# Performance work log

Hardware: AMD Instinct MI355X
Metric: run time of the kernel (lower is better)

The kernel has to match this reference:

```python
import jax, jax.numpy as jnp
import numpy as np

N, D, R, C_IN = 384, 256, 64, 2
REL_H, NEI_H = 128, 256


def setup_inputs() -> dict:
    key = jax.random.key(0)
    ks = jax.random.split(key, 16)
    inp = {
        "corr_index": jax.random.normal(ks[0], (N, N, C_IN), jnp.float32),
        "nei_index": jax.random.randint(ks[1], (N, N), 0, 2, jnp.int32),
        "nei_num": jax.random.randint(ks[2], (N,), 0, N, jnp.int32),
        "outgate": jax.random.uniform(ks[3], (N, D), jnp.float32),
        "self_h": jax.random.normal(ks[4], (N, D), jnp.float32),
        "self_c": jax.random.normal(ks[5], (N, D), jnp.float32),
        # relativeLayer: 2-layer MLP, relu after both layers (iflastac=True)
        "rel_w1": jax.random.normal(ks[6], (C_IN, REL_H), jnp.float32) * 0.1,
        "rel_b1": jnp.zeros((REL_H,), jnp.float32),
        "rel_w2": jax.random.normal(ks[7], (REL_H, R), jnp.float32) * 0.1,
        "rel_b2": jnp.zeros((R,), jnp.float32),
        # ngate: single Linear(R+2D -> D) + sigmoid
        "ngate_w": jax.random.normal(ks[8], (R + 2 * D, D), jnp.float32) * 0.005,
        "ngate_b": jnp.zeros((D,), jnp.float32),
        # WAr: single Linear(R+2D -> 1), no activation (WAr_ac='')
        "war_w": jax.random.normal(ks[9], (R + 2 * D, 1), jnp.float32) * 0.05,
        "war_b": jnp.zeros((1,), jnp.float32),
        # W_nei: Linear(D->NEI_H)+relu, Linear(NEI_H->D), no last activation
        "wnei_w1": jax.random.normal(ks[10], (D, NEI_H), jnp.float32) * 0.05,
        "wnei_b1": jnp.zeros((NEI_H,), jnp.float32),
        "wnei_w2": jax.random.normal(ks[11], (NEI_H, D), jnp.float32) * 0.05,
        "wnei_b2": jnp.zeros((D,), jnp.float32),
    }
    return inp


def reference(corr_index, nei_index, nei_num, outgate, self_h, self_c,
              rel_w1, rel_b1, rel_w2, rel_b2, ngate_w, ngate_b,
              war_w, war_b, wnei_w1, wnei_b1, wnei_w2, wnei_b2):
    n, d = self_h.shape
    mask = nei_index > 0  # [N, N], pair (i, j)
    # relativeLayer on pairwise relative coords: relu(relu(x W1 + b1) W2 + b2)
    r = jax.nn.relu(jax.nn.relu(corr_index @ rel_w1 + rel_b1) @ rel_w2 + rel_b2)  # [N,N,R]
    # In torch code flat index k = i*N + j: hi_t[k] = self_h[i], nei_inputs[k] = self_h[j]
    h_i = jnp.broadcast_to(self_h[:, None, :], (n, n, d))
    h_j = jnp.broadcast_to(self_h[None, :, :], (n, n, d))
    feat = jnp.concatenate([r, h_i, h_j], axis=-1)  # [N,N,R+2D]
    gate = jax.nn.sigmoid(feat @ ngate_w + ngate_b)  # [N,N,D]
    msg = h_j * gate
    tt = (feat @ war_w + war_b)[..., 0]  # [N,N] attention logits
    # scatter into zero-init matrix, then Pos[Pos==0] = -inf, row softmax
    pos = jnp.where(mask, tt, 0.0)
    pos = jnp.where(pos == 0.0, -jnp.inf, pos)
    pos = jax.nn.softmax(pos, axis=1)  # [N,N]
    # masked, attention-weighted messages; guard NaN from fully-masked rows
    H = jnp.where(mask[:, :, None], msg * pos[:, :, None], 0.0)  # [N,N,D]
    h_sum = jnp.sum(H, axis=1)  # [N,D]
    h_sum = jax.nn.relu(h_sum @ wnei_w1 + wnei_b1) @ wnei_w2 + wnei_b2
    C = h_sum + self_c
    H_out = outgate * jnp.tanh(C)
    return (outgate, H_out, C)
```

## Files before the change

kernel.cpp:

```cpp
#include <hip/hip_runtime.h>
#include <hip/hip_bf16.h>
#include <math.h>

#define N 384
#define D 256
#define R 64
#define RELH 128
#define NN (N*N)
#define ND (N*D)
#define JCHUNK 64
#define NCHUNK (N / JCHUNK)
#define TPB 16
#define LOG2E 1.44269504088896f

typedef _Float16 f16x8 __attribute__((ext_vector_type(8)));
typedef float f32x4 __attribute__((ext_vector_type(4)));

__device__ __forceinline__ float fast_sigmoid(float x) {
    float e = __builtin_amdgcn_exp2f(-LOG2E * x);
    return __builtin_amdgcn_rcpf(1.f + e);
}
__device__ __forceinline__ float fast_exp(float x) {
    return __builtin_amdgcn_exp2f(LOG2E * x);
}
__device__ __forceinline__ float fast_tanh(float x) {
    float e = __builtin_amdgcn_exp2f(2.f * LOG2E * x);
    return 1.f - 2.f * __builtin_amdgcn_rcpf(1.f + e);
}

__global__ __launch_bounds__(256) void prep_kernel(
        const float* __restrict__ self_h, const float* __restrict__ ngate_w,
        const float* __restrict__ war_w,
        float* __restrict__ A, float* __restrict__ Bm,
        float* __restrict__ u, float* __restrict__ v,
        _Float16* __restrict__ wf) {
    int b = blockIdx.x, tid = threadIdx.x;
    int wv = tid >> 6, l = tid & 63;
    int lg = l >> 4, ln = l & 15;

    if (b < 6) {
        int r0 = b * 64 + wv * 16;
        for (int rr = 0; rr < 16; ++rr) {
            int row = r0 + rr;
            float su = 0.f, sv = 0.f;
            #pragma unroll
            for (int k = 0; k < 4; ++k) {
                int d = k * 64 + l;
                float h = self_h[row * D + d];
                su = fmaf(h, war_w[R + d], su);
                sv = fmaf(h, war_w[R + D + d], sv);
            }
            #pragma unroll
            for (int off = 32; off; off >>= 1) {
                su += __shfl_down(su, off);
                sv += __shfl_down(sv, off);
            }
            if (l == 0) { u[row] = su; v[row] = sv; }
        }
    } else if (b < 54) {
        int W = (b - 6) * 4 + wv;
        int m0 = (W >> 3) * 16;
        int cb = (W & 7) * 64;
        const float* wsrc = ngate_w + (size_t)(cb >= 256 ? 320 : 64) * D + (cb & 255);
        f32x4 acc[4];
        #pragma unroll
        for (int nt = 0; nt < 4; ++nt) acc[nt] = (f32x4){0.f, 0.f, 0.f, 0.f};
        #pragma unroll
        for (int s = 0; s < 8; ++s) {
            const float4* hp = (const float4*)&self_h[(size_t)(m0 + ln) * D + s * 32 + lg * 8];
            float4 h0 = hp[0], h1 = hp[1];
            f16x8 af;
            af[0] = (_Float16)h0.x; af[1] = (_Float16)h0.y;
            af[2] = (_Float16)h0.z; af[3] = (_Float16)h0.w;
            af[4] = (_Float16)h1.x; af[5] = (_Float16)h1.y;
            af[6] = (_Float16)h1.z; af[7] = (_Float16)h1.w;
            #pragma unroll
            for (int nt = 0; nt < 4; ++nt) {
                f16x8 bf;
                #pragma unroll
                for (int ii = 0; ii < 8; ++ii)
                    bf[ii] = (_Float16)wsrc[(size_t)(s * 32 + lg * 8 + ii) * D + nt * 16 + ln];
                acc[nt] = __builtin_amdgcn_mfma_f32_16x16x32_f16(af, bf, acc[nt], 0, 0, 0);
            }
        }
        #pragma unroll
        for (int nt = 0; nt < 4; ++nt)
            #pragma unroll
            for (int reg = 0; reg < 4; ++reg) {
                int row = m0 + lg * 4 + reg;
                int col = cb + nt * 16 + ln;
                if (col < 256) A[row * D + col] = acc[nt][reg];
                else           Bm[row * D + (col - 256)] = acc[nt][reg];
            }
    } else {
        int blkEq = (b - 54) * 4 + wv;
        int s = blkEq >> 4, t = blkEq & 15;
        #pragma unroll
        for (int ii = 0; ii < 8; ++ii) {
            float w = ngate_w[(s * 32 + lg * 8 + ii) * D + t * 16 + ln];
            wf[((size_t)(s * 16 + t) * 64 + l) * 8 + ii] = (_Float16)w;
        }
    }
}

__global__ __launch_bounds__(384) void ttsm_kernel(
        const float* __restrict__ corr,
        const float* __restrict__ rel_w1, const float* __restrict__ rel_b1,
        const float* __restrict__ rel_w2, const float* __restrict__ rel_b2,
        const float* __restrict__ war_w, const float* __restrict__ v,
        const int* __restrict__ nei,
        float* __restrict__ pos, _Float16* __restrict__ rc) {
    __shared__ float ttrow[N];
    __shared__ float red[6];
    __shared__ float sM, sS;
    int i = blockIdx.x, tid = threadIdx.x;
    int wv = tid >> 6, l = tid & 63;
    int lg = l >> 4, ln = l & 15;

    f16x8 bfr[4][4];
    #pragma unroll
    for (int s = 0; s < 4; ++s)
        #pragma unroll
        for (int nt = 0; nt < 4; ++nt)
            #pragma unroll
            for (int ii = 0; ii < 8; ++ii)
                bfr[s][nt][ii] = (_Float16)rel_w2[(s * 32 + lg * 8 + ii) * R + nt * 16 + ln];
    float w10[4][8], w11[4][8], b1v[4][8];
    #pragma unroll
    for (int s = 0; s < 4; ++s)
        #pragma unroll
        for (int ii = 0; ii < 8; ++ii) {
            int hk = s * 32 + lg * 8 + ii;
            w10[s][ii] = rel_w1[hk];
            w11[s][ii] = rel_w1[RELH + hk];
            b1v[s][ii] = rel_b1[hk];
        }
    float b2r[4], warw[4];
    #pragma unroll
    for (int nt = 0; nt < 4; ++nt) {
        b2r[nt]  = rel_b2[nt * 16 + ln];
        warw[nt] = war_w[nt * 16 + ln];
    }

    #pragma unroll
    for (int t = 0; t < 4; ++t) {
        int j0 = wv * 64 + t * 16;
        int P0 = i * N + j0;
        float2 x = ((const float2*)corr)[P0 + ln];
        f16x8 af[4];
        #pragma unroll
        for (int s = 0; s < 4; ++s)
            #pragma unroll
            for (int ii = 0; ii < 8; ++ii) {
                float h = fmaxf(0.f, fmaf(x.y, w11[s][ii], fmaf(x.x, w10[s][ii], b1v[s][ii])));
                af[s][ii] = (_Float16)h;
            }
        f32x4 c[4];
        #pragma unroll
        for (int nt = 0; nt < 4; ++nt) c[nt] = (f32x4){0.f, 0.f, 0.f, 0.f};
        #pragma unroll
        for (int nt = 0; nt < 4; ++nt)
            #pragma unroll
            for (int s = 0; s < 4; ++s)
                c[nt] = __builtin_amdgcn_mfma_f32_16x16x32_f16(af[s], bfr[s][nt], c[nt], 0, 0, 0);
        float tpart[4] = {0.f, 0.f, 0.f, 0.f};
        #pragma unroll
        for (int nt = 0; nt < 4; ++nt)
            #pragma unroll
            for (int reg = 0; reg < 4; ++reg) {
                float rv = fmaxf(0.f, c[nt][reg] + b2r[nt]);
                int m = lg * 4 + reg;
                rc[(size_t)(P0 + m) * R + nt * 16 + ln] = (_Float16)rv;
                tpart[reg] = fmaf(rv, warw[nt], tpart[reg]);
            }
        #pragma unroll
        for (int reg = 0; reg < 4; ++reg) {
            float tsum = tpart[reg];
            #pragma unroll
            for (int off = 8; off; off >>= 1) tsum += __shfl_xor(tsum, off, 16);
            tpart[reg] = tsum;
        }
        if (ln == 0) {
            #pragma unroll
            for (int reg = 0; reg < 4; ++reg) {
                int j = j0 + lg * 4 + reg;
                ttrow[j] = tpart[reg] + v[j];
            }
        }
    }
    __syncthreads();

    float tv = ttrow[tid];
    bool va = (nei[i * N + tid] > 0) && (tv != 0.f);
    float m = va ? tv : -INFINITY;
    #pragma unroll
    for (int off = 32; off; off >>= 1) m = fmaxf(m, __shfl_down(m, off));
    if (l == 0) red[wv] = m;
    __syncthreads();
    if (tid == 0) {
        float mm = red[0];
        #pragma unroll
        for (int k = 1; k < 6; ++k) mm = fmaxf(mm, red[k]);
        sM = mm;
    }
    __syncthreads();
    float M = sM;
    float e = 0.f;
    if (va && M != -INFINITY) e = fast_exp(tv - M);
    float sum = e;
    #pragma unroll
    for (int off = 32; off; off >>= 1) sum += __shfl_down(sum, off);
    if (l == 0) red[wv] = sum;
    __syncthreads();
    if (tid == 0) {
        float ss = red[0];
        #pragma unroll
        for (int k = 1; k < 6; ++k) ss += red[k];
        sS = ss;
    }
    __syncthreads();
    float rden = (sS > 0.f) ? __builtin_amdgcn_rcpf(sS) : 0.f;
    pos[i * N + tid] = va ? e * rden : 0.f;
}

__global__ __launch_bounds__(256) void tt_valu_kernel(
        const float* __restrict__ corr,
        const float* __restrict__ rel_w1, const float* __restrict__ rel_b1,
        const float* __restrict__ rel_w2, const float* __restrict__ rel_b2,
        const float* __restrict__ war_w, const float* __restrict__ war_b,
        const float* __restrict__ u, const float* __restrict__ v,
        float* __restrict__ tt) {
    __shared__ __align__(16) float h1s[4][RELH];
    int tid = threadIdx.x, w = tid >> 6, l = tid & 63;
    float w1a0 = rel_w1[l],      w1a1 = rel_w1[RELH + l];
    float w1b0 = rel_w1[64 + l], w1b1 = rel_w1[RELH + 64 + l];
    float b1a = rel_b1[l], b1b = rel_b1[64 + l];
    float b2v = rel_b2[l], warw = war_w[l], wb = war_b[0];
    int pbase = blockIdx.x * TPB;
    #pragma unroll
    for (int it = 0; it < TPB / 4; ++it) {
        int p = pbase + it * 4 + w;
        int i = p / N, j = p - i * N;
        float2 x = *(const float2*)(corr + p * 2);
        h1s[w][l]      = fmaxf(0.f, fmaf(x.y, w1a1, fmaf(x.x, w1a0, b1a)));
        h1s[w][l + 64] = fmaxf(0.f, fmaf(x.y, w1b1, fmaf(x.x, w1b0, b1b)));
        float c0 = b2v, c1 = 0.f, c2 = 0.f, c3 = 0.f;
        const float4* hv = (const float4*)h1s[w];
        #pragma unroll
        for (int k4 = 0; k4 < RELH / 4; ++k4) {
            float4 h = hv[k4];
            c0 = fmaf(h.x, rel_w2[(k4 * 4 + 0) * R + l], c0);
            c1 = fmaf(h.y, rel_w2[(k4 * 4 + 1) * R + l], c1);
            c2 = fmaf(h.z, rel_w2[(k4 * 4 + 2) * R + l], c2);
            c3 = fmaf(h.w, rel_w2[(k4 * 4 + 3) * R + l], c3);
        }
        float rm = fmaxf(0.f, (c0 + c1) + (c2 + c3));
        float part = rm * warw;
        for (int off = 32; off; off >>= 1) part += __shfl_down(part, off);
        if (l == 0) tt[p] = part + u[i] + v[j] + wb;
    }
}

__global__ void softmax_kernel(const float* __restrict__ tt,
                               const int* __restrict__ nei,
                               float* __restrict__ pos) {
    __shared__ float red[4];
    __shared__ float sM, sS;
    int i = blockIdx.x, tid = threadIdx.x;
    float tv[2]; bool valid[2];
    float m = -INFINITY;
    for (int s = 0; s < 2; ++s) {
        int j = tid + s * 256;
        valid[s] = false; tv[s] = 0.f;
        if (j < N) {
            float t = tt[i * N + j];
            bool va = (nei[i * N + j] > 0) && (t != 0.f);
            tv[s] = t; valid[s] = va;
            if (va) m = fmaxf(m, t);
        }
    }
    for (int off = 32; off; off >>= 1) m = fmaxf(m, __shfl_down(m, off));
    if ((tid & 63) == 0) red[tid >> 6] = m;
    __syncthreads();
    if (tid == 0) sM = fmaxf(fmaxf(red[0], red[1]), fmaxf(red[2], red[3]));
    __syncthreads();
    float M = sM;
    float e[2] = {0.f, 0.f};
    float sum = 0.f;
    if (M != -INFINITY) {
        for (int s = 0; s < 2; ++s)
            if (valid[s]) { e[s] = fast_exp(tv[s] - M); sum += e[s]; }
    }
    for (int off = 32; off; off >>= 1) sum += __shfl_down(sum, off);
    if ((tid & 63) == 0) red[tid >> 6] = sum;
    __syncthreads();
    if (tid == 0) sS = red[0] + red[1] + red[2] + red[3];
    __syncthreads();
    float rden = (sS > 0.f) ? __builtin_amdgcn_rcpf(sS) : 0.f;
    for (int s = 0; s < 2; ++s) {
        int j = tid + s * 256;
        if (j < N) pos[i * N + j] = valid[s] ? e[s] * rden : 0.f;
    }
}

__global__ __launch_bounds__(256, 2) void gate_mfma_kernel(
        const _Float16* __restrict__ rc16, const _Float16* __restrict__ wf,
        const float* __restrict__ ngate_b, const float* __restrict__ A,
        const float* __restrict__ Bm, const float* __restrict__ pos,
        const float* __restrict__ self_h, float* __restrict__ partial) {
    int i = blockIdx.x;
    int jbase = blockIdx.y * JCHUNK;
    int tid = threadIdx.x, w = tid >> 6, l = tid & 63;
    int lg = l >> 4, ln = l & 15;

    f16x8 bf[2][4];
    #pragma unroll
    for (int s = 0; s < 2; ++s)
        #pragma unroll
        for (int t = 0; t < 4; ++t)
            bf[s][t] = *(const f16x8*)&wf[((size_t)(s * 16 + w * 4 + t) * 64 + l) * 8];

    f16x8 af[4][2];
    #pragma unroll
    for (int jt = 0; jt < 4; ++jt)
        #pragma unroll
        for (int s = 0; s < 2; ++s)
            af[jt][s] = *(const f16x8*)&rc16[(size_t)(i * N + jbase + jt * 16 + ln) * R + s * 32 + lg * 8];

    float pj[4][4];
    #pragma unroll
    for (int jt = 0; jt < 4; ++jt)
        #pragma unroll
        for (int reg = 0; reg < 4; ++reg)
            pj[jt][reg] = pos[i * N + jbase + jt * 16 + lg * 4 + reg];

    float based[4];
    #pragma unroll
    for (int t = 0; t < 4; ++t) {
        int d = w * 64 + t * 16 + ln;
        based[t] = ngate_b[d] + A[i * D + d];
    }

    float acc[4] = {0.f, 0.f, 0.f, 0.f};
    #pragma unroll
    for (int jt = 0; jt < 4; ++jt) {
        f32x4 c[4];
        #pragma unroll
        for (int t = 0; t < 4; ++t) {
            int d = w * 64 + t * 16 + ln;
            #pragma unroll
            for (int reg = 0; reg < 4; ++reg)
                c[t][reg] = Bm[(size_t)(jbase + jt * 16 + lg * 4 + reg) * D + d];
        }
        #pragma unroll
        for (int t = 0; t < 4; ++t)
            #pragma unroll
            for (int s = 0; s < 2; ++s)
                c[t] = __builtin_amdgcn_mfma_f32_16x16x32_f16(af[jt][s], bf[s][t], c[t], 0, 0, 0);
        #pragma unroll
        for (int reg = 0; reg < 4; ++reg) {
            int jj = jbase + jt * 16 + lg * 4 + reg;
            float p = pj[jt][reg];
            #pragma unroll
            for (int t = 0; t < 4; ++t) {
                int d = w * 64 + t * 16 + ln;
                float h  = self_h[jj * D + d];
                float g = fast_sigmoid(c[t][reg] + based[t]);
                acc[t] = fmaf(p * h, g, acc[t]);
            }
        }
    }
    #pragma unroll
    for (int t = 0; t < 4; ++t) {
        float a = acc[t];
        a += __shfl_xor(a, 16);
        a += __shfl_xor(a, 32);
        acc[t] = a;
    }
    if (lg == 0) {
        #pragma unroll
        for (int t = 0; t < 4; ++t)
            partial[(size_t)(blockIdx.y * N + i) * D + w * 64 + t * 16 + ln] = acc[t];
    }
}

__global__ void gate_norc_kernel(const float* __restrict__ corr,
                            const float* __restrict__ rel_w1, const float* __restrict__ rel_b1,
                            const float* __restrict__ rel_w2, const float* __restrict__ rel_b2,
                            const float* __restrict__ ngate_w, const float* __restrict__ ngate_b,
                            const float* __restrict__ A, const float* __restrict__ Bm,
                            const float* __restrict__ pos, const float* __restrict__ self_h,
                            float* __restrict__ partial) {
    __shared__ __align__(16) float h1[4][RELH];
    __shared__ __align__(16) float rs[4][R];
    __shared__ float wsh[4];
    int i = blockIdx.x, tid = threadIdx.x;
    int jbase = blockIdx.y * JCHUNK;
    int w = tid >> 6, l = tid & 63;
    ((float*)rs)[tid] = 0.f;
    float base = ngate_b[tid] + A[i * D + tid];
    float acc = 0.f;
    for (int j0 = jbase; j0 < jbase + JCHUNK; j0 += 4) {
        int j = j0 + w;
        int p = i * N + j;
        float wt = pos[p];
        if (l == 0) wsh[w] = wt;
        if (wt != 0.f) {
            float x0 = corr[p * 2], x1 = corr[p * 2 + 1];
            h1[w][l]      = fmaxf(0.f, fmaf(x1, rel_w1[RELH + l],      fmaf(x0, rel_w1[l],      rel_b1[l])));
            h1[w][l + 64] = fmaxf(0.f, fmaf(x1, rel_w1[RELH + l + 64], fmaf(x0, rel_w1[l + 64], rel_b1[l + 64])));
        }
        __syncthreads();
        if (wsh[w] != 0.f) {
            float c0 = rel_b2[l], c1 = 0.f, c2 = 0.f, c3 = 0.f;
            const float4* hv = (const float4*)h1[w];
            #pragma unroll 8
            for (int k4 = 0; k4 < RELH / 4; ++k4) {
                float4 h = hv[k4];
                int k = k4 * 4;
                c0 = fmaf(h.x, rel_w2[k * R + l], c0);
                c1 = fmaf(h.y, rel_w2[(k + 1) * R + l], c1);
                c2 = fmaf(h.z, rel_w2[(k + 2) * R + l], c2);
                c3 = fmaf(h.w, rel_w2[(k + 3) * R + l], c3);
            }
            rs[w][l] = fmaxf(0.f, (c0 + c1) + (c2 + c3));
        }
        __syncthreads();
        #pragma unroll
        for (int ww = 0; ww < 4; ++ww) {
            float wtj = wsh[ww];
            if (wtj != 0.f) {
                int jj = j0 + ww;
                const float4* rv = (const float4*)rs[ww];
                float l0 = 0.f, l1 = 0.f, l2 = 0.f, l3 = 0.f;
                #pragma unroll 4
                for (int m4 = 0; m4 < R / 4; ++m4) {
                    float4 r4 = rv[m4];
                    int m = m4 * 4;
                    l0 = fmaf(r4.x, ngate_w[m * D + tid], l0);
                    l1 = fmaf(r4.y, ngate_w[(m + 1) * D + tid], l1);
                    l2 = fmaf(r4.z, ngate_w[(m + 2) * D + tid], l2);
                    l3 = fmaf(r4.w, ngate_w[(m + 3) * D + tid], l3);
                }
                float logit = base + Bm[jj * D + tid] + ((l0 + l1) + (l2 + l3));
                float g = fast_sigmoid(logit);
                acc = fmaf(wtj * self_h[jj * D + tid], g, acc);
            }
        }
        __syncthreads();
    }
    partial[(blockIdx.y * N + i) * D + tid] = acc;
}

__global__ void final_kernel(const float* __restrict__ partial,
                             const float* __restrict__ wnei_w1, const float* __restrict__ wnei_b1,
                             const float* __restrict__ wnei_w2, const float* __restrict__ wnei_b2,
                             const float* __restrict__ self_c, const float* __restrict__ outgate,
                             float* __restrict__ out) {
    __shared__ __align__(16) float hs[D];
    __shared__ __align__(16) float hid[D];
    int i = blockIdx.x, d = threadIdx.x;
    float s = 0.f;
    #pragma unroll
    for (int c = 0; c < NCHUNK; ++c) s += partial[(c * N + i) * D + d];
    hs[d] = s;
    __syncthreads();
    float a0 = wnei_b1[d], a1 = 0.f, a2 = 0.f, a3 = 0.f;
    const float4* hv = (const float4*)hs;
    #pragma unroll 4
    for (int t4 = 0; t4 < D / 4; ++t4) {
        float4 h = hv[t4];
        int t = t4 * 4;
        a0 = fmaf(h.x, wnei_w1[t * D + d], a0);
        a1 = fmaf(h.y, wnei_w1[(t + 1) * D + d], a1);
        a2 = fmaf(h.z, wnei_w1[(t + 2) * D + d], a2);
        a3 = fmaf(h.w, wnei_w1[(t + 3) * D + d], a3);
    }
    hid[d] = fmaxf(0.f, (a0 + a1) + (a2 + a3));
    __syncthreads();
    float b0 = wnei_b2[d], b1 = 0.f, b2 = 0.f, b3 = 0.f;
    const float4* gv = (const float4*)hid;
    #pragma unroll 4
    for (int t4 = 0; t4 < D / 4; ++t4) {
        float4 h = gv[t4];
        int t = t4 * 4;
        b0 = fmaf(h.x, wnei_w2[t * D + d], b0);
        b1 = fmaf(h.y, wnei_w2[(t + 1) * D + d], b1);
        b2 = fmaf(h.z, wnei_w2[(t + 2) * D + d], b2);
        b3 = fmaf(h.w, wnei_w2[(t + 3) * D + d], b3);
    }
    int idx = i * D + d;
    float C = (b0 + b1) + (b2 + b3) + self_c[idx];
    float og = outgate[idx];
    out[idx] = og;
    out[ND + idx] = og * fast_tanh(C);
    out[2 * ND + idx] = C;
}

extern "C" void kernel_launch(void* const* d_in, const int* in_sizes, int n_in,
                              void* d_out, int out_size, void* d_ws, size_t ws_size,
                              hipStream_t stream) {
    const float* corr    = (const float*)d_in[0];
    const int*   nei     = (const int*)d_in[1];
    const float* outg    = (const float*)d_in[3];
    const float* self_h  = (const float*)d_in[4];
    const float* self_c  = (const float*)d_in[5];
    const float* rel_w1  = (const float*)d_in[6];
    const float* rel_b1  = (const float*)d_in[7];
    const float* rel_w2  = (const float*)d_in[8];
    const float* rel_b2  = (const float*)d_in[9];
    const float* ngate_w = (const float*)d_in[10];
    const float* ngate_b = (const float*)d_in[11];
    const float* war_w   = (const float*)d_in[12];
    const float* war_b   = (const float*)d_in[13];
    const float* wnei_w1 = (const float*)d_in[14];
    const float* wnei_b1 = (const float*)d_in[15];
    const float* wnei_w2 = (const float*)d_in[16];
    const float* wnei_b2 = (const float*)d_in[17];

    float* ws      = (float*)d_ws;
    float* tt      = ws;
    float* pos     = ws + NN;
    float* A       = ws + 2 * NN;
    float* Bm      = ws + 2 * NN + ND;
    float* u       = ws + 2 * NN + 2 * ND;
    float* v       = u + N;
    float* partial = v + N;
    float* tail    = partial + NCHUNK * ND;
    _Float16* rc16 = (_Float16*)tail;
    _Float16* wf   = rc16 + (size_t)NN * R;
    size_t base_floats = (size_t)(2 * NN + 2 * ND + 2 * N + NCHUNK * ND);
    size_t need = (base_floats + ((size_t)NN * R + 2 * 16 * 64 * 8) / 2 + 16) * sizeof(float);
    bool use_rc = ws_size >= need;
    float* out = (float*)d_out;

    prep_kernel<<<62, 256, 0, stream>>>(self_h, ngate_w, war_w, A, Bm, u, v, wf);
    if (use_rc) {
        ttsm_kernel<<<N, 384, 0, stream>>>(corr, rel_w1, rel_b1, rel_w2, rel_b2,
                                           war_w, v, nei, pos, rc16);
        dim3 ggrid(N, NCHUNK);
        gate_mfma_kernel<<<ggrid, 256, 0, stream>>>(rc16, wf, ngate_b, A, Bm, pos, self_h,
                                                    partial);
    } else {
        tt_valu_kernel<<<NN / TPB, 256, 0, stream>>>(corr, rel_w1, rel_b1, rel_w2, rel_b2,
                                                     war_w, war_b, u, v, tt);
        softmax_kernel<<<N, 256, 0, stream>>>(tt, nei, pos);
        dim3 ggrid(N, NCHUNK);
        gate_norc_kernel<<<ggrid, 256, 0, stream>>>(corr, rel_w1, rel_b1, rel_w2, rel_b2,
                                                    ngate_w, ngate_b, A, Bm, pos, self_h,
                                                    partial);
    }
    final_kernel<<<N, 256, 0, stream>>>(partial, wnei_w1, wnei_b1, wnei_w2, wnei_b2,
                                        self_c, outg, out);
}
```

Baseline: 71.23 us.

## Retile gate kernel over i-tiles with shared packed Bm/self_h, batch final rows

The gate kernel now has each block process four i rows (one per wave) over half of D. The j-chunk's Bm and self_h values are packed as fp16 pairs in prep and staged once into LDS, so all four waves reuse them instead of each reloading fp32 Bm and self_h from global memory. ngate_b is folded into A during prep. The MFMA accumulator now starts from zero, with the packed Bm added in fp32. The final MLP kernel handles four rows per block, so each weight load is reused four times. The costs are reduced precision on Bm and self_h, more registers per thread, and LDS usage.

After: 89.84 us. 1.26x slower.

```diff
diff --git a/kernel.cpp b/kernel.cpp
--- a/kernel.cpp
+++ b/kernel.cpp
@@ -12,8 +12,10 @@
 #define NCHUNK (N / JCHUNK)
 #define TPB 16
 #define LOG2E 1.44269504088896f
+#define BHS_STRIDE 132
 
 typedef _Float16 f16x8 __attribute__((ext_vector_type(8)));
+typedef _Float16 f16x2 __attribute__((ext_vector_type(2)));
 typedef float f32x4 __attribute__((ext_vector_type(4)));
 
 __device__ __forceinline__ float fast_sigmoid(float x) {
@@ -30,8 +32,9 @@
 
 __global__ __launch_bounds__(256) void prep_kernel(
         const float* __restrict__ self_h, const float* __restrict__ ngate_w,
-        const float* __restrict__ war_w,
+        const float* __restrict__ ngate_b, const float* __restrict__ war_w,
         float* __restrict__ A, float* __restrict__ Bm,
+        unsigned int* __restrict__ bh,
         float* __restrict__ u, float* __restrict__ v,
         _Float16* __restrict__ wf) {
     int b = blockIdx.x, tid = threadIdx.x;
@@ -89,8 +92,17 @@
             for (int reg = 0; reg < 4; ++reg) {
                 int row = m0 + lg * 4 + reg;
                 int col = cb + nt * 16 + ln;
-                if (col < 256) A[row * D + col] = acc[nt][reg];
-                else           Bm[row * D + (col - 256)] = acc[nt][reg];
+                if (col < 256) {
+                    A[row * D + col] = acc[nt][reg] + ngate_b[col];
+                } else {
+                    int c2 = col - 256;
+                    float bmv = acc[nt][reg];
+                    Bm[row * D + c2] = bmv;
+                    f16x2 pk;
+                    pk[0] = (_Float16)bmv;
+                    pk[1] = (_Float16)self_h[row * D + c2];
+                    bh[row * D + c2] = __builtin_bit_cast(unsigned int, pk);
+                }
             }
     } else {
         int blkEq = (b - 54) * 4 + wv;
@@ -305,27 +317,37 @@
 
 __global__ __launch_bounds__(256, 2) void gate_mfma_kernel(
         const _Float16* __restrict__ rc16, const _Float16* __restrict__ wf,
-        const float* __restrict__ ngate_b, const float* __restrict__ A,
-        const float* __restrict__ Bm, const float* __restrict__ pos,
-        const float* __restrict__ self_h, float* __restrict__ partial) {
-    int i = blockIdx.x;
-    int jbase = blockIdx.y * JCHUNK;
-    int tid = threadIdx.x, w = tid >> 6, l = tid & 63;
+        const float* __restrict__ A, const unsigned int* __restrict__ bh,
+        const float* __restrict__ pos, float* __restrict__ partial) {
+    __shared__ unsigned int bhs[64 * BHS_STRIDE];
+    int itile = blockIdx.x, jc = blockIdx.y, dh = blockIdx.z;
+    int jbase = jc * JCHUNK;
+    int tid = threadIdx.x, wv = tid >> 6, l = tid & 63;
     int lg = l >> 4, ln = l & 15;
-
-    f16x8 bf[2][4];
+    int i = itile * 4 + wv;
+
+    {
+        const uint4* src = (const uint4*)bh;
+        #pragma unroll
+        for (int s = 0; s < 8; ++s) {
+            int f4 = tid + s * 256;
+            int row = f4 >> 5, c4 = f4 & 31;
+            uint4 vv = src[(size_t)(jbase + row) * (D / 4) + dh * 32 + c4];
+            *(uint4*)&bhs[row * BHS_STRIDE + c4 * 4] = vv;
+        }
+    }
+
+    f16x8 bf[2][8];
     #pragma unroll
     for (int s = 0; s < 2; ++s)
         #pragma unroll
-        for (int t = 0; t < 4; ++t)
-            bf[s][t] = *(const f16x8*)&wf[((size_t)(s * 16 + w * 4 + t) * 64 + l) * 8];
-
-    f16x8 af[4][2];
-    #pragma unroll
-    for (int jt = 0; jt < 4; ++jt)
-        #pragma unroll
-        for (int s = 0; s < 2; ++s)
-            af[jt][s] = *(const f16x8*)&rc16[(size_t)(i * N + jbase + jt * 16 + ln) * R + s * 32 + lg * 8];
+        for (int dt = 0; dt < 8; ++dt)
+            bf[s][dt] = *(const f16x8*)&wf[((size_t)(s * 16 + dh * 8 + dt) * 64 + l) * 8];
+
+    float based[8];
+    #pragma unroll
+    for (int dt = 0; dt < 8; ++dt)
+        based[dt] = A[i * D + dh * 128 + dt * 16 + ln];
 
     float pj[4][4];
     #pragma unroll
@@ -334,60 +356,55 @@
         for (int reg = 0; reg < 4; ++reg)
             pj[jt][reg] = pos[i * N + jbase + jt * 16 + lg * 4 + reg];
 
-    float based[4];
-    #pragma unroll
-    for (int t = 0; t < 4; ++t) {
-        int d = w * 64 + t * 16 + ln;
-        based[t] = ngate_b[d] + A[i * D + d];
-    }
-
-    float acc[4] = {0.f, 0.f, 0.f, 0.f};
+    __syncthreads();
+
+    float acc[8] = {0.f, 0.f, 0.f, 0.f, 0.f, 0.f, 0.f, 0.f};
     #pragma unroll
     for (int jt = 0; jt < 4; ++jt) {
-        f32x4 c[4];
-        #pragma unroll
-        for (int t = 0; t < 4; ++t) {
-            int d = w * 64 + t * 16 + ln;
-            #pragma unroll
-            for (int reg = 0; reg < 4; ++reg)
-                c[t][reg] = Bm[(size_t)(jbase + jt * 16 + lg * 4 + reg) * D + d];
-        }
-        #pragma unroll
-        for (int t = 0; t < 4; ++t)
+        f16x8 af[2];
+        #pragma unroll
+        for (int s = 0; s < 2; ++s)
+            af[s] = *(const f16x8*)&rc16[(size_t)(i * N + jbase + jt * 16 + ln) * R + s * 32 + lg * 8];
+        f32x4 c[8];
+        #pragma unroll
+        for (int dt = 0; dt < 8; ++dt) c[dt] = (f32x4){0.f, 0.f, 0.f, 0.f};
+        #pragma unroll
+        for (int dt = 0; dt < 8; ++dt)
             #pragma unroll
             for (int s = 0; s < 2; ++s)
-                c[t] = __builtin_amdgcn_mfma_f32_16x16x32_f16(af[jt][s], bf[s][t], c[t], 0, 0, 0);
+                c[dt] = __builtin_amdgcn_mfma_f32_16x16x32_f16(af[s], bf[s][dt], c[dt], 0, 0, 0);
         #pragma unroll
         for (int reg = 0; reg < 4; ++reg) {
-            int jj = jbase + jt * 16 + lg * 4 + reg;
+            int jl = jt * 16 + lg * 4 + reg;
             float p = pj[jt][reg];
             #pragma unroll
-            for (int t = 0; t < 4; ++t) {
-                int d = w * 64 + t * 16 + ln;
-                float h  = self_h[jj * D + d];
-                float g = fast_sigmoid(c[t][reg] + based[t]);
-                acc[t] = fmaf(p * h, g, acc[t]);
-            }
-        }
-    }
-    #pragma unroll
-    for (int t = 0; t < 4; ++t) {
-        float a = acc[t];
+            for (int dt = 0; dt < 8; ++dt) {
+                unsigned int uu = bhs[jl * BHS_STRIDE + dt * 16 + ln];
+                f16x2 bhv = __builtin_bit_cast(f16x2, uu);
+                float logit = c[dt][reg] + based[dt] + (float)bhv[0];
+                float g = fast_sigmoid(logit);
+                acc[dt] = fmaf(p * g, (float)bhv[1], acc[dt]);
+            }
+        }
+    }
+    #pragma unroll
+    for (int dt = 0; dt < 8; ++dt) {
+        float a = acc[dt];
         a += __shfl_xor(a, 16);
         a += __shfl_xor(a, 32);
-        acc[t] = a;
+        acc[dt] = a;
     }
     if (lg == 0) {
         #pragma unroll
-        for (int t = 0; t < 4; ++t)
-            partial[(size_t)(blockIdx.y * N + i) * D + w * 64 + t * 16 + ln] = acc[t];
+        for (int dt = 0; dt < 8; ++dt)
+            partial[(size_t)(jc * N + i) * D + dh * 128 + dt * 16 + ln] = acc[dt];
     }
 }
 
 __global__ void gate_norc_kernel(const float* __restrict__ corr,
                             const float* __restrict__ rel_w1, const float* __restrict__ rel_b1,
                             const float* __restrict__ rel_w2, const float* __restrict__ rel_b2,
-                            const float* __restrict__ ngate_w, const float* __restrict__ ngate_b,
+                            const float* __restrict__ ngate_w,
                             const float* __restrict__ A, const float* __restrict__ Bm,
                             const float* __restrict__ pos, const float* __restrict__ self_h,
                             float* __restrict__ partial) {
@@ -398,7 +415,7 @@
     int jbase = blockIdx.y * JCHUNK;
     int w = tid >> 6, l = tid & 63;
     ((float*)rs)[tid] = 0.f;
-    float base = ngate_b[tid] + A[i * D + tid];
+    float base = A[i * D + tid];
     float acc = 0.f;
     for (int j0 = jbase; j0 < jbase + JCHUNK; j0 += 4) {
         int j = j0 + w;
@@ -452,49 +469,55 @@
     partial[(blockIdx.y * N + i) * D + tid] = acc;
 }
 
-__global__ void final_kernel(const float* __restrict__ partial,
-                             const float* __restrict__ wnei_w1, const float* __restrict__ wnei_b1,
-                             const float* __restrict__ wnei_w2, const float* __restrict__ wnei_b2,
-                             const float* __restrict__ self_c, const float* __restrict__ outgate,
-                             float* __restrict__ out) {
-    __shared__ __align__(16) float hs[D];
-    __shared__ __align__(16) float hid[D];
-    int i = blockIdx.x, d = threadIdx.x;
-    float s = 0.f;
-    #pragma unroll
-    for (int c = 0; c < NCHUNK; ++c) s += partial[(c * N + i) * D + d];
-    hs[d] = s;
-    __syncthreads();
-    float a0 = wnei_b1[d], a1 = 0.f, a2 = 0.f, a3 = 0.f;
-    const float4* hv = (const float4*)hs;
-    #pragma unroll 4
-    for (int t4 = 0; t4 < D / 4; ++t4) {
-        float4 h = hv[t4];
-        int t = t4 * 4;
-        a0 = fmaf(h.x, wnei_w1[t * D + d], a0);
-        a1 = fmaf(h.y, wnei_w1[(t + 1) * D + d], a1);
-        a2 = fmaf(h.z, wnei_w1[(t + 2) * D + d], a2);
-        a3 = fmaf(h.w, wnei_w1[(t + 3) * D + d], a3);
-    }
-    hid[d] = fmaxf(0.f, (a0 + a1) + (a2 + a3));
-    __syncthreads();
-    float b0 = wnei_b2[d], b1 = 0.f, b2 = 0.f, b3 = 0.f;
-    const float4* gv = (const float4*)hid;
-    #pragma unroll 4
-    for (int t4 = 0; t4 < D / 4; ++t4) {
-        float4 h = gv[t4];
-        int t = t4 * 4;
-        b0 = fmaf(h.x, wnei_w2[t * D + d], b0);
-        b1 = fmaf(h.y, wnei_w2[(t + 1) * D + d], b1);
-        b2 = fmaf(h.z, wnei_w2[(t + 2) * D + d], b2);
-        b3 = fmaf(h.w, wnei_w2[(t + 3) * D + d], b3);
-    }
-    int idx = i * D + d;
-    float C = (b0 + b1) + (b2 + b3) + self_c[idx];
-    float og = outgate[idx];
-    out[idx] = og;
-    out[ND + idx] = og * fast_tanh(C);
-    out[2 * ND + idx] = C;
+__global__ __launch_bounds__(256) void final_kernel(
+        const float* __restrict__ partial,
+        const float* __restrict__ wnei_w1, const float* __restrict__ wnei_b1,
+        const float* __restrict__ wnei_w2, const float* __restrict__ wnei_b2,
+        const float* __restrict__ self_c, const float* __restrict__ outgate,
+        float* __restrict__ out) {
+    __shared__ __align__(16) float hs[4][D];
+    __shared__ __align__(16) float hid[4][D];
+    int i0 = blockIdx.x * 4, d = threadIdx.x;
+    #pragma unroll
+    for (int r = 0; r < 4; ++r) {
+        float s = 0.f;
+        #pragma unroll
+        for (int c = 0; c < NCHUNK; ++c) s += partial[(size_t)(c * N + i0 + r) * D + d];
+        hs[r][d] = s;
+    }
+    __syncthreads();
+    {
+        float b1 = wnei_b1[d];
+        float a[4] = {b1, b1, b1, b1};
+        #pragma unroll 4
+        for (int t = 0; t < D; ++t) {
+            float w = wnei_w1[t * D + d];
+            #pragma unroll
+            for (int r = 0; r < 4; ++r) a[r] = fmaf(hs[r][t], w, a[r]);
+        }
+        #pragma unroll
+        for (int r = 0; r < 4; ++r) hid[r][d] = fmaxf(0.f, a[r]);
+    }
+    __syncthreads();
+    {
+        float b2 = wnei_b2[d];
+        float bacc[4] = {b2, b2, b2, b2};
+        #pragma unroll 4
+        for (int t = 0; t < D; ++t) {
+            float w = wnei_w2[t * D + d];
+            #pragma unroll
+            for (int r = 0; r < 4; ++r) bacc[r] = fmaf(hid[r][t], w, bacc[r]);
+        }
+        #pragma unroll
+        for (int r = 0; r < 4; ++r) {
+            int idx = (i0 + r) * D + d;
+            float C = bacc[r] + self_c[idx];
+            float og = outgate[idx];
+            out[idx] = og;
+            out[ND + idx] = og * fast_tanh(C);
+            out[2 * ND + idx] = C;
+        }
+    }
 }
 
 extern "C" void kernel_launch(void* const* d_in, const int* in_sizes, int n_in,
@@ -526,30 +549,31 @@
     float* u       = ws + 2 * NN + 2 * ND;
     float* v       = u + N;
     float* partial = v + N;
-    float* tail    = partial + NCHUNK * ND;
+    unsigned int* bh = (unsigned int*)(partial + NCHUNK * ND);
+    float* tail    = (float*)(bh + ND);
     _Float16* rc16 = (_Float16*)tail;
     _Float16* wf   = rc16 + (size_t)NN * R;
-    size_t base_floats = (size_t)(2 * NN + 2 * ND + 2 * N + NCHUNK * ND);
+    size_t base_floats = (size_t)(2 * NN + 3 * ND + 2 * N + NCHUNK * ND);
     size_t need = (base_floats + ((size_t)NN * R + 2 * 16 * 64 * 8) / 2 + 16) * sizeof(float);
     bool use_rc = ws_size >= need;
     float* out = (float*)d_out;
 
-    prep_kernel<<<62, 256, 0, stream>>>(self_h, ngate_w, war_w, A, Bm, u, v, wf);
+    prep_kernel<<<62, 256, 0, stream>>>(self_h, ngate_w, ngate_b, war_w,
+                                        A, Bm, bh, u, v, wf);
     if (use_rc) {
         ttsm_kernel<<<N, 384, 0, stream>>>(corr, rel_w1, rel_b1, rel_w2, rel_b2,
                                            war_w, v, nei, pos, rc16);
-        dim3 ggrid(N, NCHUNK);
-        gate_mfma_kernel<<<ggrid, 256, 0, stream>>>(rc16, wf, ngate_b, A, Bm, pos, self_h,
-                                                    partial);
+        dim3 ggrid(N / 4, NCHUNK, 2);
+        gate_mfma_kernel<<<ggrid, 256, 0, stream>>>(rc16, wf, A, bh, pos, partial);
     } else {
         tt_valu_kernel<<<NN / TPB, 256, 0, stream>>>(corr, rel_w1, rel_b1, rel_w2, rel_b2,
                                                      war_w, war_b, u, v, tt);
         softmax_kernel<<<N, 256, 0, stream>>>(tt, nei, pos);
         dim3 ggrid(N, NCHUNK);
         gate_norc_kernel<<<ggrid, 256, 0, stream>>>(corr, rel_w1, rel_b1, rel_w2, rel_b2,
-                                                    ngate_w, ngate_b, A, Bm, pos, self_h,
+                                                    ngate_w, A, Bm, pos, self_h,
                                                     partial);
     }
-    final_kernel<<<N, 256, 0, stream>>>(partial, wnei_w1, wnei_b1, wnei_w2, wnei_b2,
-                                        self_c, outg, out);
-}
+    final_kernel<<<N / 4, 256, 0, stream>>>(partial, wnei_w1, wnei_b1, wnei_w2, wnei_b2,
+                                            self_c, outg, out);
+}
```
